# Kernel optimization log

Measured on AMD Instinct MI355X. Metric: run time of the kernel, lower is better.

The kernel has to match this reference:

```python
import jax, jax.numpy as jnp
import numpy as np

S = 2048        # seq_len (number of rigid bodies)
D = 256         # node_dim
H = 16          # num_heads
C = 64          # num_channels
SPATIAL_DIM = 3
QUATERNION_DIM = 4


def setup_inputs() -> dict:
    key = jax.random.key(0)
    ks = jax.random.split(key, 9)
    nodes = jax.random.normal(ks[0], (S, D), jnp.float32)
    pos = jax.random.normal(ks[1], (S, 2 * SPATIAL_DIM), jnp.float32)
    rot = jax.random.normal(ks[2], (S, QUATERNION_DIM), jnp.float32)
    w = 0.02
    Wn = jax.random.normal(ks[3], (2 * H * C, D), jnp.float32) * w
    bn = jnp.zeros((2 * H * C,), jnp.float32)
    Wp = jax.random.normal(ks[4], (2 * H * C, 2 * SPATIAL_DIM), jnp.float32) * w
    bp = jnp.zeros((2 * H * C,), jnp.float32)
    Wr = jax.random.normal(ks[5], (2 * H * C, QUATERNION_DIM), jnp.float32) * w  # no bias
    Wv = jax.random.normal(ks[6], (3 * H * D, D), jnp.float32) * w
    bv = jnp.zeros((3 * H * D,), jnp.float32)
    return {"nodes": nodes, "pos": pos, "rot": rot,
            "Wn": Wn, "bn": bn, "Wp": Wp, "bp": bp, "Wr": Wr,
            "Wv": Wv, "bv": bv}


def _kq(x, W, b):
    # eqx.nn.Linear: y = W @ x + b, vmapped over seq -> x @ W.T + b
    y = x @ W.T
    if b is not None:
        y = y + b
    y = y.reshape(x.shape[0], H, 2 * C)
    k, q = jnp.split(y, 2, axis=-1)  # each (S, H, C)
    return k, q


def reference(nodes, pos, rot, Wn, bn, Wp, bp, Wr, Wv, bv):
    seq_len = nodes.shape[0]
    nodes_k, nodes_q = _kq(nodes, Wn, bn)
    pos_k, pos_q = _kq(pos, Wp, bp)
    rot_k, rot_q = _kq(rot, Wr, None)
    k = jnp.concatenate([nodes_k, pos_k, rot_k], axis=-2)  # (S, 3H, C)
    q = jnp.concatenate([nodes_q, pos_q, rot_q], axis=-2)  # (S, 3H, C)
    val = (nodes @ Wv.T + bv).reshape(seq_len, 3 * H, D)   # (S, 3H, D)
    logits = jnp.einsum('ihc,jhc->ijh', k, q)              # (S, S, 3H)
    # square the rotation-source logits (last H of the 3H head axis)
    logits = logits.at[..., -H:].set(jnp.square(logits[..., -H:]))
    logits = logits / jnp.sqrt(jnp.float32(H))
    att = jax.nn.softmax(logits, axis=-2)                  # softmax over key axis j
    out = jnp.einsum('ijh,jhd->id', att, val)              # (S, D)
    return out
```

## Files before the change

kernel.cpp:

```cpp
#include <hip/hip_runtime.h>
#include <hip/hip_bf16.h>

typedef __bf16 bf16;
typedef __attribute__((ext_vector_type(8)))  __bf16 bf16x8;
typedef __attribute__((ext_vector_type(4)))  __bf16 bf16x4;
typedef __attribute__((ext_vector_type(4)))  float  f32x4;

#define SEQ   2048
#define NDIM  256
#define NH3   48
#define CH    64
#define SQS   72
#define SVS   72
#define SPS   72
#define VTS   2176

#define OFF_NODES 0
#define OFF_POS   524288
#define OFF_ROT   536576
#define OFF_WN    544768
#define OFF_BN    1069056
#define OFF_WP    1071104
#define OFF_BP    1083392
#define OFF_WR    1085440
#define OFF_WV    1093632
#define OFF_BV    4239360
#define TOT_IN    4251648

__device__ bf16  g_in[TOT_IN];
__device__ bf16  g_k [NH3 * SEQ * CH];
__device__ bf16  g_q [NH3 * SEQ * CH];
__device__ bf16  g_vt[NH3 * NDIM * VTS];
__device__ float g_part[(size_t)NH3 * SEQ * NDIM];
__device__ int   g_isf32;

__global__ __launch_bounds__(256) void detect_k(const unsigned short* __restrict__ p) {
    __shared__ int cff, czero;
    if (threadIdx.x == 0) { cff = 0; czero = 0; }
    __syncthreads();
    int ff = 0, zz = 0;
    for (int r = 0; r < 64; ++r) {
        int idx = threadIdx.x * 64 + r;
        unsigned short u = p[idx];
        if (((u >> 7) & 0xFF) == 0xFF) ff++;
        if (((idx & 1) == 0) && (u == 0)) zz++;
    }
    if (ff) atomicAdd(&cff, ff);
    if (zz) atomicAdd(&czero, zz);
    __syncthreads();
    if (threadIdx.x == 0) g_isf32 = (cff > 2 || czero > 6000) ? 1 : 0;
}

__global__ __launch_bounds__(256) void convert_k(
    const void* s0, const void* s1, const void* s2, const void* s3, const void* s4,
    const void* s5, const void* s6, const void* s7, const void* s8, const void* s9)
{
    const void* srcs[10] = {s0, s1, s2, s3, s4, s5, s6, s7, s8, s9};
    const int   szs[10]  = {524288, 12288, 8192, 524288, 2048, 12288, 2048, 8192, 3145728, 12288};
    const int   offs[10] = {OFF_NODES, OFF_POS, OFF_ROT, OFF_WN, OFF_BN,
                            OFF_WP, OFF_BP, OFF_WR, OFF_WV, OFF_BV};
    const int y = blockIdx.y;
    const void* src = srcs[y];
    bf16* dst = g_in + offs[y];
    const int n = szs[y];
    const int isf = g_isf32;
    const int stride = gridDim.x * 256 * 4;
    for (int i = (blockIdx.x * 256 + threadIdx.x) * 4; i < n; i += stride) {
        bf16x4 o;
        if (isf) {
            float4 v = *(const float4*)((const float*)src + i);
            o[0] = (bf16)v.x; o[1] = (bf16)v.y; o[2] = (bf16)v.z; o[3] = (bf16)v.w;
        } else {
            o = *(const bf16x4*)((const bf16*)src + i);
        }
        *(bf16x4*)(dst + i) = o;
    }
}

__global__ __launch_bounds__(256) void proj_nodes_kq()
{
    __shared__ __align__(16) bf16 sB[64 * 264];
    const bf16* nodes = g_in + OFF_NODES;
    const bf16* Wn    = g_in + OFF_WN;
    const bf16* bn    = g_in + OFF_BN;
    const int t    = threadIdx.x;
    const int bx   = blockIdx.x;
    const int xcd  = bx & 7;
    const int rest = bx >> 3;
    const int f0   = (xcd * 4 + (rest & 3)) * 64;
    const int s0   = (rest >> 2) * 64;

    for (int rep = 0; rep < 8; ++rep) {
        int idx = t + rep * 256;
        int row = idx >> 5, chunk = idx & 31;
        *(bf16x8*)&sB[row * 264 + chunk * 8] =
            *(const bf16x8*)&Wn[(f0 + row) * 256 + chunk * 8];
    }
    __syncthreads();

    const int w = t >> 6, lane = t & 63;
    const int l15 = lane & 15, quad = lane >> 4;

    f32x4 acc[4] = {{}, {}, {}, {}};
    const bf16* arow = nodes + (s0 + w * 16 + l15) * 256 + quad * 8;
#pragma unroll
    for (int kc = 0; kc < 8; ++kc) {
        bf16x8 af = *(const bf16x8*)(arow + kc * 32);
#pragma unroll
        for (int ft = 0; ft < 4; ++ft) {
            bf16x8 bfr = *(const bf16x8*)&sB[(ft * 16 + l15) * 264 + kc * 32 + quad * 8];
            acc[ft] = __builtin_amdgcn_mfma_f32_16x16x32_bf16(af, bfr, acc[ft], 0, 0, 0);
        }
    }
#pragma unroll
    for (int ft = 0; ft < 4; ++ft) {
        int f = f0 + ft * 16 + l15;
        float bias = (float)bn[f];
        int h = f >> 7, c2 = f & 127;
        bf16* base = (c2 < 64) ? (g_k + h * SEQ * CH + c2)
                               : (g_q + h * SEQ * CH + (c2 - 64));
#pragma unroll
        for (int r = 0; r < 4; ++r) {
            int s = s0 + w * 16 + quad * 4 + r;
            base[s * CH] = (bf16)(acc[ft][r] + bias);
        }
    }
}

__global__ __launch_bounds__(256) void proj_posrot_kq()
{
    const bf16* pos  = g_in + OFF_POS;
    const bf16* rotq = g_in + OFF_ROT;
    const bf16* Wp   = g_in + OFF_WP;
    const bf16* bp   = g_in + OFF_BP;
    const bf16* Wr   = g_in + OFF_WR;
    int id = blockIdx.x * 256 + threadIdx.x;
    int fg  = id & 511;
    int s   = (id >> 9) & 2047;
    int src = id >> 20;
    int f0  = fg * 4;
    float y[4]; int h;
    if (src == 0) {
#pragma unroll
        for (int j = 0; j < 4; ++j) {
            float a = (float)bp[f0 + j];
#pragma unroll
            for (int x = 0; x < 6; ++x)
                a += (float)pos[s * 6 + x] * (float)Wp[(f0 + j) * 6 + x];
            y[j] = a;
        }
        h = 16 + (f0 >> 7);
    } else {
#pragma unroll
        for (int j = 0; j < 4; ++j) {
            float a = 0.f;
#pragma unroll
            for (int x = 0; x < 4; ++x)
                a += (float)rotq[s * 4 + x] * (float)Wr[(f0 + j) * 4 + x];
            y[j] = a;
        }
        h = 32 + (f0 >> 7);
    }
    bf16x4 o;
#pragma unroll
    for (int j = 0; j < 4; ++j) o[j] = (bf16)y[j];
    int c2 = f0 & 127;
    if (c2 < 64) *(bf16x4*)&g_k[(h * SEQ + s) * CH + c2]        = o;
    else         *(bf16x4*)&g_q[(h * SEQ + s) * CH + (c2 - 64)] = o;
}

__global__ __launch_bounds__(256) void proj_v()
{
    __shared__ __align__(16) bf16 sB[64 * 264];
    __shared__ __align__(16) bf16 sO[64 * 72];
    const bf16* nodes = g_in + OFF_NODES;
    const bf16* Wv    = g_in + OFF_WV;
    const bf16* bv    = g_in + OFF_BV;
    const int t    = threadIdx.x;
    const int bx   = blockIdx.x;
    const int xcd  = bx & 7;
    const int rest = bx >> 3;
    const int f0   = (xcd * 24 + (rest % 24)) * 64;
    const int s0   = (rest / 24) * 64;

    for (int rep = 0; rep < 8; ++rep) {
        int idx = t + rep * 256;
        int row = idx >> 5, chunk = idx & 31;
        *(bf16x8*)&sB[row * 264 + chunk * 8] =
            *(const bf16x8*)&Wv[(size_t)(f0 + row) * 256 + chunk * 8];
    }
    __syncthreads();

    const int w = t >> 6, lane = t & 63;
    const int l15 = lane & 15, quad = lane >> 4;

    f32x4 acc[4] = {{}, {}, {}, {}};
    const bf16* arow = nodes + (s0 + w * 16 + l15) * 256 + quad * 8;
#pragma unroll
    for (int kc = 0; kc < 8; ++kc) {
        bf16x8 af = *(const bf16x8*)(arow + kc * 32);
#pragma unroll
        for (int ft = 0; ft < 4; ++ft) {
            bf16x8 bfr = *(const bf16x8*)&sB[(ft * 16 + l15) * 264 + kc * 32 + quad * 8];
            acc[ft] = __builtin_amdgcn_mfma_f32_16x16x32_bf16(af, bfr, acc[ft], 0, 0, 0);
        }
    }
    __syncthreads();
#pragma unroll
    for (int ft = 0; ft < 4; ++ft) {
        int n = f0 + ft * 16 + l15;
        float bias = (float)bv[n];
#pragma unroll
        for (int r = 0; r < 4; ++r) {
            sO[(ft * 16 + l15) * 72 + (quad * 4 + r) * 4 + w] = (bf16)(acc[ft][r] + bias);
        }
    }
    __syncthreads();
    for (int rep = 0; rep < 2; ++rep) {
        int idx = t + rep * 256;
        int row = idx >> 3, chunk = idx & 7;
        *(bf16x8*)&g_vt[(size_t)(f0 + row) * VTS + s0 + chunk * 8] =
            *(const bf16x8*)&sO[row * 72 + chunk * 8];
    }
}

__global__ __launch_bounds__(512, 4) void attn_k()
{
    const int bx  = blockIdx.x;
    const int xcd = bx & 7;
    const int sub = bx >> 3;
    const int h   = xcd * 6 + (sub % 6);
    const int it  = sub / 6;
    const int i0  = it * 128;
    const int t   = threadIdx.x;
    const int w   = t >> 6, lane = t & 63;
    const int l15 = lane & 15, quad = lane >> 4;
    const bool rot = (h >= 32);

    __shared__ __align__(16) bf16 sQ[64 * SQS];
    __shared__ __align__(16) bf16 sV[256 * SVS];
    __shared__ __align__(16) bf16 sP[128 * SPS];
    __shared__ float sL[128];

    const bf16* kb = g_k  + h * SEQ * CH;
    const bf16* qb = g_q  + h * SEQ * CH;
    const bf16* vb = g_vt + (size_t)h * NDIM * VTS;

    bf16x8 kf0 = *(const bf16x8*)&kb[(i0 + w * 16 + l15) * CH + quad * 8];
    bf16x8 kf1 = *(const bf16x8*)&kb[(i0 + w * 16 + l15) * CH + 32 + quad * 8];

    const int ih = w >> 2, dq = w & 3;

    const int qrow = t >> 3, qch = t & 7;

    f32x4 acc[4][4];
#pragma unroll
    for (int a = 0; a < 4; ++a)
#pragma unroll
        for (int b = 0; b < 4; ++b) acc[a][b] = (f32x4){0.f, 0.f, 0.f, 0.f};
    f32x4 lp = {0.f, 0.f, 0.f, 0.f};

    bf16x8 qpre, vpre[4];
    qpre = *(const bf16x8*)&qb[t * 8];
#pragma unroll
    for (int rep = 0; rep < 4; ++rep) {
        int idx = t + rep * 512;
        vpre[rep] = *(const bf16x8*)&vb[(size_t)(idx >> 3) * VTS + (idx & 7) * 8];
    }
    *(bf16x8*)&sQ[qrow * SQS + qch * 8] = qpre;
#pragma unroll
    for (int rep = 0; rep < 4; ++rep) {
        int idx = t + rep * 512;
        *(bf16x8*)&sV[(idx >> 3) * SVS + (idx & 7) * 8] = vpre[rep];
    }
    __syncthreads();

    for (int st = 0; st < 32; ++st) {
        f32x4 sjb[4];
#pragma unroll
        for (int jb = 0; jb < 4; ++jb) {
            bf16x8 q0 = *(const bf16x8*)&sQ[(jb * 16 + l15) * SQS + quad * 8];
            bf16x8 q1 = *(const bf16x8*)&sQ[(jb * 16 + l15) * SQS + 32 + quad * 8];
            f32x4 sa = {};
            sa = __builtin_amdgcn_mfma_f32_16x16x32_bf16(kf0, q0, sa, 0, 0, 0);
            sa = __builtin_amdgcn_mfma_f32_16x16x32_bf16(kf1, q1, sa, 0, 0, 0);
            sjb[jb] = sa;
        }

#pragma unroll
        for (int r = 0; r < 4; ++r) {
            bf16x4 pk;
#pragma unroll
            for (int jb = 0; jb < 4; ++jb) {
                float d = sjb[jb][r];
                float x = rot ? (d * d * 0.25f) : (d * 0.25f);
                x = fminf(x, 60.f);
                float p = __expf(x);
                lp[r] += p;
                pk[jb] = (bf16)p;
            }
            *(bf16x4*)&sP[(w * 16 + quad * 4 + r) * SPS + l15 * 4] = pk;
        }
        __syncthreads();

        if (st < 31) {
            const bf16* qn = qb + (st + 1) * 4096;
            const bf16* vn = vb + (st + 1) * 64;
            qpre = *(const bf16x8*)&qn[t * 8];
#pragma unroll
            for (int rep = 0; rep < 4; ++rep) {
                int idx = t + rep * 512;
                vpre[rep] = *(const bf16x8*)&vn[(size_t)(idx >> 3) * VTS + (idx & 7) * 8];
            }
        }

#pragma unroll
        for (int kc = 0; kc < 2; ++kc) {
            bf16x8 ap[4], vf[4];
#pragma unroll
            for (int itr = 0; itr < 4; ++itr)
                ap[itr] = *(const bf16x8*)&sP[(ih * 64 + itr * 16 + l15) * SPS + kc * 32 + quad * 8];
#pragma unroll
            for (int dt = 0; dt < 4; ++dt)
                vf[dt] = *(const bf16x8*)&sV[(dq * 64 + dt * 16 + l15) * SVS + kc * 32 + quad * 8];
#pragma unroll
            for (int itr = 0; itr < 4; ++itr)
#pragma unroll
                for (int dt = 0; dt < 4; ++dt)
                    acc[itr][dt] = __builtin_amdgcn_mfma_f32_16x16x32_bf16(
                        ap[itr], vf[dt], acc[itr][dt], 0, 0, 0);
        }
        __syncthreads();

        if (st < 31) {
            *(bf16x8*)&sQ[qrow * SQS + qch * 8] = qpre;
#pragma unroll
            for (int rep = 0; rep < 4; ++rep) {
                int idx = t + rep * 512;
                *(bf16x8*)&sV[(idx >> 3) * SVS + (idx & 7) * 8] = vpre[rep];
            }
            __syncthreads();
        }
    }

#pragma unroll
    for (int off = 1; off < 16; off <<= 1) {
#pragma unroll
        for (int r = 0; r < 4; ++r) lp[r] += __shfl_xor(lp[r], off, 64);
    }
    if (l15 == 0) *(f32x4*)&sL[w * 16 + quad * 4] = lp;
    __syncthreads();

    float* pb = g_part + (size_t)h * SEQ * NDIM;
#pragma unroll
    for (int itr = 0; itr < 4; ++itr) {
        f32x4 lv = *(const f32x4*)&sL[ih * 64 + itr * 16 + quad * 4];
#pragma unroll
        for (int r = 0; r < 4; ++r) {
            float inv = 1.0f / lv[r];
            float* ob = &pb[(size_t)(i0 + ih * 64 + itr * 16 + quad * 4 + r) * NDIM + dq * 64 + l15];
#pragma unroll
            for (int dt = 0; dt < 4; ++dt)
                ob[dt * 16] = acc[itr][dt][r] * inv;
        }
    }
}

__global__ __launch_bounds__(256) void finalize_k(float* __restrict__ out) {
    int idx = (blockIdx.x * 256 + threadIdx.x) * 4;
    f32x4 s = {0.f, 0.f, 0.f, 0.f};
#pragma unroll
    for (int hh = 0; hh < NH3; ++hh)
        s += *(const f32x4*)&g_part[(size_t)hh * SEQ * NDIM + idx];
    *(f32x4*)&out[idx] = s;
}

extern "C" void kernel_launch(void* const* d_in, const int* in_sizes, int n_in,
                              void* d_out, int out_size, void* d_ws, size_t ws_size,
                              hipStream_t stream) {
    detect_k <<<dim3(1),        dim3(256), 0, stream>>>((const unsigned short*)d_in[8]);
    convert_k<<<dim3(768, 10),  dim3(256), 0, stream>>>(d_in[0], d_in[1], d_in[2], d_in[3],
                                                        d_in[4], d_in[5], d_in[6], d_in[7],
                                                        d_in[8], d_in[9]);
    proj_nodes_kq <<<dim3(1024),  dim3(256), 0, stream>>>();
    proj_posrot_kq<<<dim3(8192),  dim3(256), 0, stream>>>();
    proj_v        <<<dim3(6144),  dim3(256), 0, stream>>>();
    attn_k        <<<dim3(768),   dim3(512), 0, stream>>>();
    finalize_k    <<<dim3(512),   dim3(256), 0, stream>>>((float*)d_out);
}
```

Before: 334.9 us.

## Load V fragments directly from global and double-buffer Q/P in shared memory

V tiles are no longer staged through shared memory. Each wave reads its MFMA V operands straight from global memory (L2/L1), and Q and P become double-buffered so each iteration needs one barrier instead of three. This cuts LDS traffic, LDS footprint and synchronisation. In exchange, V global reads are duplicated across the two i-halves of waves, and global load latency now sits directly in front of the PV MFMAs.

```diff
diff --git a/kernel.cpp b/kernel.cpp
--- a/kernel.cpp
+++ b/kernel.cpp
@@ -237,9 +237,8 @@
     const int l15 = lane & 15, quad = lane >> 4;
     const bool rot = (h >= 32);
 
-    __shared__ __align__(16) bf16 sQ[64 * SQS];
-    __shared__ __align__(16) bf16 sV[256 * SVS];
-    __shared__ __align__(16) bf16 sP[128 * SPS];
+    __shared__ __align__(16) bf16 sQ[2][64 * SQS];
+    __shared__ __align__(16) bf16 sP[2][128 * SPS];
     __shared__ float sL[128];
 
     const bf16* kb = g_k  + h * SEQ * CH;
@@ -253,6 +252,8 @@
 
     const int qrow = t >> 3, qch = t & 7;
 
+    const bf16* vbase = vb + (size_t)(dq * 64 + l15) * VTS + quad * 8;
+
     f32x4 acc[4][4];
 #pragma unroll
     for (int a = 0; a < 4; ++a)
@@ -260,27 +261,19 @@
         for (int b = 0; b < 4; ++b) acc[a][b] = (f32x4){0.f, 0.f, 0.f, 0.f};
     f32x4 lp = {0.f, 0.f, 0.f, 0.f};
 
-    bf16x8 qpre, vpre[4];
-    qpre = *(const bf16x8*)&qb[t * 8];
-#pragma unroll
-    for (int rep = 0; rep < 4; ++rep) {
-        int idx = t + rep * 512;
-        vpre[rep] = *(const bf16x8*)&vb[(size_t)(idx >> 3) * VTS + (idx & 7) * 8];
-    }
-    *(bf16x8*)&sQ[qrow * SQS + qch * 8] = qpre;
-#pragma unroll
-    for (int rep = 0; rep < 4; ++rep) {
-        int idx = t + rep * 512;
-        *(bf16x8*)&sV[(idx >> 3) * SVS + (idx & 7) * 8] = vpre[rep];
-    }
+    *(bf16x8*)&sQ[0][qrow * SQS + qch * 8] = *(const bf16x8*)&qb[t * 8];
     __syncthreads();
 
     for (int st = 0; st < 32; ++st) {
+        const int cur = st & 1;
+        const bf16* sQc = sQ[cur];
+        bf16*       sPc = sP[cur];
+
         f32x4 sjb[4];
 #pragma unroll
         for (int jb = 0; jb < 4; ++jb) {
-            bf16x8 q0 = *(const bf16x8*)&sQ[(jb * 16 + l15) * SQS + quad * 8];
-            bf16x8 q1 = *(const bf16x8*)&sQ[(jb * 16 + l15) * SQS + 32 + quad * 8];
+            bf16x8 q0 = *(const bf16x8*)&sQc[(jb * 16 + l15) * SQS + quad * 8];
+            bf16x8 q1 = *(const bf16x8*)&sQc[(jb * 16 + l15) * SQS + 32 + quad * 8];
             f32x4 sa = {};
             sa = __builtin_amdgcn_mfma_f32_16x16x32_bf16(kf0, q0, sa, 0, 0, 0);
             sa = __builtin_amdgcn_mfma_f32_16x16x32_bf16(kf1, q1, sa, 0, 0, 0);
@@ -299,48 +292,45 @@
                 lp[r] += p;
                 pk[jb] = (bf16)p;
             }
-            *(bf16x4*)&sP[(w * 16 + quad * 4 + r) * SPS + l15 * 4] = pk;
-        }
+            *(bf16x4*)&sPc[(w * 16 + quad * 4 + r) * SPS + l15 * 4] = pk;
+        }
+
+        if (st < 31)
+            *(bf16x8*)&sQ[cur ^ 1][qrow * SQS + qch * 8] =
+                *(const bf16x8*)&qb[(st + 1) * 4096 + t * 8];
+
+        const bf16* vs = vbase + st * 64;
+        bf16x8 vf0[4];
+#pragma unroll
+        for (int dt = 0; dt < 4; ++dt)
+            vf0[dt] = *(const bf16x8*)&vs[(size_t)dt * (16 * VTS)];
+
         __syncthreads();
 
-        if (st < 31) {
-            const bf16* qn = qb + (st + 1) * 4096;
-            const bf16* vn = vb + (st + 1) * 64;
-            qpre = *(const bf16x8*)&qn[t * 8];
-#pragma unroll
-            for (int rep = 0; rep < 4; ++rep) {
-                int idx = t + rep * 512;
-                vpre[rep] = *(const bf16x8*)&vn[(size_t)(idx >> 3) * VTS + (idx & 7) * 8];
-            }
-        }
-
-#pragma unroll
-        for (int kc = 0; kc < 2; ++kc) {
-            bf16x8 ap[4], vf[4];
-#pragma unroll
-            for (int itr = 0; itr < 4; ++itr)
-                ap[itr] = *(const bf16x8*)&sP[(ih * 64 + itr * 16 + l15) * SPS + kc * 32 + quad * 8];
+        bf16x8 ap0[4];
+#pragma unroll
+        for (int itr = 0; itr < 4; ++itr)
+            ap0[itr] = *(const bf16x8*)&sPc[(ih * 64 + itr * 16 + l15) * SPS + quad * 8];
+        bf16x8 vf1[4];
+#pragma unroll
+        for (int dt = 0; dt < 4; ++dt)
+            vf1[dt] = *(const bf16x8*)&vs[(size_t)dt * (16 * VTS) + 32];
+#pragma unroll
+        for (int itr = 0; itr < 4; ++itr)
 #pragma unroll
             for (int dt = 0; dt < 4; ++dt)
-                vf[dt] = *(const bf16x8*)&sV[(dq * 64 + dt * 16 + l15) * SVS + kc * 32 + quad * 8];
-#pragma unroll
-            for (int itr = 0; itr < 4; ++itr)
-#pragma unroll
-                for (int dt = 0; dt < 4; ++dt)
-                    acc[itr][dt] = __builtin_amdgcn_mfma_f32_16x16x32_bf16(
-                        ap[itr], vf[dt], acc[itr][dt], 0, 0, 0);
-        }
-        __syncthreads();
-
-        if (st < 31) {
-            *(bf16x8*)&sQ[qrow * SQS + qch * 8] = qpre;
-#pragma unroll
-            for (int rep = 0; rep < 4; ++rep) {
-                int idx = t + rep * 512;
-                *(bf16x8*)&sV[(idx >> 3) * SVS + (idx & 7) * 8] = vpre[rep];
-            }
-            __syncthreads();
-        }
+                acc[itr][dt] = __builtin_amdgcn_mfma_f32_16x16x32_bf16(
+                    ap0[itr], vf0[dt], acc[itr][dt], 0, 0, 0);
+        bf16x8 ap1[4];
+#pragma unroll
+        for (int itr = 0; itr < 4; ++itr)
+            ap1[itr] = *(const bf16x8*)&sPc[(ih * 64 + itr * 16 + l15) * SPS + 32 + quad * 8];
+#pragma unroll
+        for (int itr = 0; itr < 4; ++itr)
+#pragma unroll
+            for (int dt = 0; dt < 4; ++dt)
+                acc[itr][dt] = __builtin_amdgcn_mfma_f32_16x16x32_bf16(
+                    ap1[itr], vf1[dt], acc[itr][dt], 0, 0, 0);
     }
 
 #pragma unroll
```

After: 396.9 us. 1.19x slower.
